# Performance work log

Measured on AMD Instinct MI355X. Metric: run time of the kernel, lower is better.

The kernel has to match this reference:

```python
import jax, jax.numpy as jnp
import numpy as np

NUM_HEADS = 8


def setup_inputs() -> dict:
    key = jax.random.key(0)
    ks = jax.random.split(key, 6)
    S, B, L, E = 4, 4, 4096, 1024
    scale = 1.0 / np.sqrt(E)
    return {
        "stream_outputs": jax.random.normal(ks[0], (S, B, L, E), dtype=jnp.float32),
        "stream_query": jax.random.normal(ks[1], (1, 1, E), dtype=jnp.float32),
        "in_proj_weight": jax.random.uniform(ks[2], (3 * E, E), dtype=jnp.float32, minval=-scale, maxval=scale),
        "in_proj_bias": jnp.zeros((3 * E,), dtype=jnp.float32),
        "out_proj_weight": jax.random.uniform(ks[3], (E, E), dtype=jnp.float32, minval=-scale, maxval=scale),
        "out_proj_bias": jnp.zeros((E,), dtype=jnp.float32),
    }


def reference(stream_outputs, stream_query, in_proj_weight, in_proj_bias,
              out_proj_weight, out_proj_bias):
    S, B, L, E = stream_outputs.shape
    H = NUM_HEADS
    D = E // H
    scale = 1.0 / jnp.sqrt(jnp.asarray(D, dtype=stream_outputs.dtype))

    Wq, Wk, Wv = in_proj_weight[:E], in_proj_weight[E:2 * E], in_proj_weight[2 * E:]
    bq, bk, bv = in_proj_bias[:E], in_proj_bias[E:2 * E], in_proj_bias[2 * E:]

    # query is identical for every token: project once -> [H, D]
    q = (stream_query[0, 0] @ Wq.T + bq).reshape(H, D)

    # streams as KV: [B, L, S, E]
    x = jnp.transpose(stream_outputs, (1, 2, 0, 3))
    k = (jnp.einsum('blse,fe->blsf', x, Wk) + bk).reshape(B, L, S, H, D)
    v = (jnp.einsum('blse,fe->blsf', x, Wv) + bv).reshape(B, L, S, H, D)

    logits = jnp.einsum('hd,blshd->blhs', q, k) * scale  # [B, L, H, S]
    attn = jax.nn.softmax(logits, axis=-1)

    ctx = jnp.einsum('blhs,blshd->blhd', attn, v).reshape(B, L, E)
    aggregated = jnp.einsum('ble,fe->blf', ctx, out_proj_weight) + out_proj_bias

    # torch MHA returns attn weights averaged over heads -> [B, L, S] -> [S, B, L]
    weights = jnp.transpose(jnp.mean(attn, axis=2), (2, 0, 1))
    return aggregated, weights
```

## Files before the change

kernel.cpp:

```cpp
#include <hip/hip_runtime.h>
#include <hip/hip_bf16.h>
#include <math.h>

#define SS 4
#define BB 4
#define LL 4096
#define EE 1024
#define HH 8
#define DD 128
#define TT (BB*LL)
#define AGG_ELEMS ((long)TT*EE)

using bf16  = __hip_bfloat16;
using bfp2  = __hip_bfloat162;
using bhalf8_t  = __attribute__((ext_vector_type(8))) short;
using floatx4_t = __attribute__((ext_vector_type(4))) float;

__device__ __forceinline__ void gload16(const void* g, void* l) {
  __builtin_amdgcn_global_load_lds((const __attribute__((address_space(1))) void*)g,
                                   (__attribute__((address_space(3))) void*)l, 16, 0, 0);
}

__global__ __launch_bounds__(256) void k_convert(const float* __restrict__ Wv,
                                                 const float* __restrict__ Wo,
                                                 bf16* __restrict__ WvB,
                                                 bf16* __restrict__ WoB) {
  int i = blockIdx.x * 256 + threadIdx.x;
  float4 a = ((const float4*)Wv)[i];
  float4 b = ((const float4*)Wo)[i];
  bfp2 p;
  p.x = __float2bfloat16(a.x); p.y = __float2bfloat16(a.y); ((bfp2*)WvB)[2*i]   = p;
  p.x = __float2bfloat16(a.z); p.y = __float2bfloat16(a.w); ((bfp2*)WvB)[2*i+1] = p;
  p.x = __float2bfloat16(b.x); p.y = __float2bfloat16(b.y); ((bfp2*)WoB)[2*i]   = p;
  p.x = __float2bfloat16(b.z); p.y = __float2bfloat16(b.w); ((bfp2*)WoB)[2*i+1] = p;
}

__global__ __launch_bounds__(256) void k_q(const float* __restrict__ query,
                                           const float* __restrict__ Wq,
                                           const float* __restrict__ bq,
                                           float* __restrict__ q) {
  int lane = threadIdx.x & 63;
  int f = blockIdx.x * 4 + (threadIdx.x >> 6);
  const float* wr = Wq + (long)f * EE;
  float acc = 0.f;
  for (int e = lane; e < EE; e += 64) acc += query[e] * wr[e];
#pragma unroll
  for (int o = 32; o; o >>= 1) acc += __shfl_down(acc, o);
  if (!lane) q[f] = acc + bq[f];
}

__global__ __launch_bounds__(256) void k_qk(const float* __restrict__ q,
                                            const float* __restrict__ Wk,
                                            float* __restrict__ qk) {
  int idx = blockIdx.x * 256 + threadIdx.x;
  int h = idx >> 10, e = idx & 1023;
  const float* qh = q + h * DD;
  float acc = 0.f;
  for (int d = 0; d < DD; ++d) acc += qh[d] * Wk[(long)(h * DD + d) * EE + e];
  qk[idx] = acc * 0.088388347648318447f;
}

__global__ __launch_bounds__(256) void k_attn_y(const float* __restrict__ X,
                                                const float* __restrict__ qk,
                                                float* __restrict__ attn_ws,
                                                float* __restrict__ wout,
                                                bf16* __restrict__ y,
                                                int h0, int hc, int doAttn) {
  __shared__ float xs[16][EE];
  int tid = threadIdx.x;
  long tok0 = (long)blockIdx.x * 4;
#pragma unroll
  for (int it = 0; it < 16; ++it) {
    int j = it * 256 + tid;
    int row = j >> 8, c4 = j & 255;
    long tok = tok0 + (row >> 2);
    int s = row & 3;
    const float4* src = (const float4*)(X + ((long)s * TT + tok) * EE) + c4;
    *(float4*)&xs[row][c4 * 4] = *src;
  }
  __syncthreads();

  int wave = tid >> 6, lane = tid & 63;
  long tok = tok0 + wave;
  int r0 = wave * 4;
  float attn[HH][SS];

  if (doAttn) {
    float acc[HH][SS];
#pragma unroll
    for (int h = 0; h < HH; ++h)
#pragma unroll
      for (int s = 0; s < SS; ++s) acc[h][s] = 0.f;
    for (int i = 0; i < 16; ++i) {
      int e = i * 64 + lane;
      float xv[SS];
#pragma unroll
      for (int s = 0; s < SS; ++s) xv[s] = xs[r0 + s][e];
#pragma unroll
      for (int h = 0; h < HH; ++h) {
        float qv = qk[h * EE + e];
#pragma unroll
        for (int s = 0; s < SS; ++s) acc[h][s] += qv * xv[s];
      }
    }
#pragma unroll
    for (int h = 0; h < HH; ++h)
#pragma unroll
      for (int s = 0; s < SS; ++s)
#pragma unroll
        for (int o = 1; o < 64; o <<= 1) acc[h][s] += __shfl_xor(acc[h][s], o);
#pragma unroll
    for (int h = 0; h < HH; ++h) {
      float m = fmaxf(fmaxf(acc[h][0], acc[h][1]), fmaxf(acc[h][2], acc[h][3]));
      float p0 = __expf(acc[h][0] - m), p1 = __expf(acc[h][1] - m);
      float p2 = __expf(acc[h][2] - m), p3 = __expf(acc[h][3] - m);
      float inv = 1.f / (p0 + p1 + p2 + p3);
      attn[h][0] = p0 * inv; attn[h][1] = p1 * inv;
      attn[h][2] = p2 * inv; attn[h][3] = p3 * inv;
    }
    if (lane == 0) {
#pragma unroll
      for (int h = 0; h < HH; ++h)
#pragma unroll
        for (int s = 0; s < SS; ++s) attn_ws[tok * 32 + h * 4 + s] = attn[h][s];
#pragma unroll
      for (int s = 0; s < SS; ++s) {
        float wsum = 0.125f * (attn[0][s] + attn[1][s] + attn[2][s] + attn[3][s] +
                               attn[4][s] + attn[5][s] + attn[6][s] + attn[7][s]);
        wout[(long)s * TT + tok] = wsum;
      }
    }
  } else {
#pragma unroll
    for (int h = 0; h < HH; ++h)
#pragma unroll
      for (int s = 0; s < SS; ++s) attn[h][s] = attn_ws[tok * 32 + h * 4 + s];
  }

#pragma unroll
  for (int h = 0; h < HH; ++h) {
    if (h < h0 || h >= h0 + hc) continue;
    float a0 = attn[h][0], a1 = attn[h][1], a2 = attn[h][2], a3 = attn[h][3];
    bf16* yr = y + ((long)(h - h0) * TT + tok) * EE;
#pragma unroll
    for (int i = 0; i < 8; ++i) {
      int e = i * 128 + lane * 2;
      float2 v0 = *(const float2*)&xs[r0][e];
      float2 v1 = *(const float2*)&xs[r0 + 1][e];
      float2 v2 = *(const float2*)&xs[r0 + 2][e];
      float2 v3 = *(const float2*)&xs[r0 + 3][e];
      float u0 = a0 * v0.x + a1 * v1.x + a2 * v2.x + a3 * v3.x;
      float u1 = a0 * v0.y + a1 * v1.y + a2 * v2.y + a3 * v3.y;
      bfp2 pk; pk.x = __float2bfloat16(u0); pk.y = __float2bfloat16(u1);
      *(bfp2*)&yr[e] = pk;
    }
  }
}

template <bool OUTF32>
__global__ __launch_bounds__(256) void k_gemm128(const bf16* __restrict__ A,
                                                 const bf16* __restrict__ Bt,
                                                 const float* __restrict__ bias,
                                                 void* __restrict__ C,
                                                 int K, int ldc, int nbase0,
                                                 long aStrideY, long btStrideY) {
  __shared__ bf16 As[128 * 64];
  __shared__ bf16 Bs[128 * 64];
  A  += (long)blockIdx.y * aStrideY;
  Bt += (long)blockIdx.y * btStrideY;
  int tid = threadIdx.x, wave = tid >> 6, lane = tid & 63;
  long m0 = (long)blockIdx.x * 128;
  int wm = wave >> 1, wn = wave & 1;
  floatx4_t acc[4][4];
#pragma unroll
  for (int i = 0; i < 4; ++i)
#pragma unroll
    for (int j = 0; j < 4; ++j) acc[i][j] = (floatx4_t){0.f, 0.f, 0.f, 0.f};

  int lrow = lane >> 3;
  int lcol = (lane & 7) * 8;

  for (int k0 = 0; k0 < K; k0 += 64) {
#pragma unroll
    for (int i = 0; i < 4; ++i) {
      int seg = wave * 4 + i;
      int row = seg * 8 + lrow;
      gload16(A  + (m0 + row) * (long)K + k0 + lcol, &As[seg * 512]);
      gload16(Bt + (long)row * K        + k0 + lcol, &Bs[seg * 512]);
    }
    __syncthreads();
#pragma unroll
    for (int kk = 0; kk < 2; ++kk) {
      bhalf8_t af[4], bfr[4];
#pragma unroll
      for (int mi = 0; mi < 4; ++mi) {
        int m = wm * 64 + mi * 16 + (lane & 15);
        af[mi] = *(const bhalf8_t*)&As[m * 64 + kk * 32 + (lane >> 4) * 8];
      }
#pragma unroll
      for (int ni = 0; ni < 4; ++ni) {
        int n = wn * 64 + ni * 16 + (lane & 15);
        bfr[ni] = *(const bhalf8_t*)&Bs[n * 64 + kk * 32 + (lane >> 4) * 8];
      }
#pragma unroll
      for (int mi = 0; mi < 4; ++mi)
#pragma unroll
        for (int ni = 0; ni < 4; ++ni)
          acc[mi][ni] = __builtin_amdgcn_mfma_f32_16x16x32_bf16(af[mi], bfr[ni], acc[mi][ni], 0, 0, 0);
    }
    __syncthreads();
  }

  int cl = lane & 15, rg = (lane >> 4) * 4;
#pragma unroll
  for (int mi = 0; mi < 4; ++mi) {
    long trow = m0 + wm * 64 + mi * 16 + rg;
#pragma unroll
    for (int ni = 0; ni < 4; ++ni) {
      int n = nbase0 + blockIdx.y * 128 + wn * 64 + ni * 16 + cl;
      float bv = bias[n];
#pragma unroll
      for (int r = 0; r < 4; ++r) {
        float v = acc[mi][ni][r] + bv;
        if (OUTF32) ((float*)C)[(trow + r) * (long)ldc + n] = v;
        else        ((bf16*)C)[(trow + r) * (long)ldc + n] = __float2bfloat16(v);
      }
    }
  }
}

extern "C" void kernel_launch(void* const* d_in, const int* in_sizes, int n_in,
                              void* d_out, int out_size, void* d_ws, size_t ws_size,
                              hipStream_t stream) {
  const float* SO  = (const float*)d_in[0];
  const float* SQ  = (const float*)d_in[1];
  const float* IPW = (const float*)d_in[2];
  const float* IPB = (const float*)d_in[3];
  const float* OPW = (const float*)d_in[4];
  const float* OPB = (const float*)d_in[5];
  float* out = (float*)d_out;
  char* ws = (char*)d_ws;

  size_t off = 0;
  auto alloc = [&](size_t bytes) -> void* {
    void* p = ws + off;
    off = (off + bytes + 255) & ~(size_t)255;
    return p;
  };
  float* q    = (float*)alloc((size_t)EE * 4);
  float* qk   = (float*)alloc((size_t)HH * EE * 4);
  float* attn = (float*)alloc((size_t)TT * 32 * 4);
  bf16*  WvB  = (bf16*) alloc((size_t)EE * EE * 2);
  bf16*  WoB  = (bf16*) alloc((size_t)EE * EE * 2);
  bf16*  ctxB = (bf16*) alloc((size_t)TT * EE * 2);
  int HC = HH;
  while (HC > 1 && off + (size_t)TT * HC * EE * 2 > ws_size) HC >>= 1;
  bf16* y = (bf16*)(ws + off);

  k_convert<<<EE * EE / 1024, 256, 0, stream>>>(IPW + 2 * EE * EE, OPW, WvB, WoB);
  k_q<<<EE / 4, 256, 0, stream>>>(SQ, IPW, IPB, q);
  k_qk<<<HH * EE / 256, 256, 0, stream>>>(q, IPW + EE * EE, qk);

  for (int h0 = 0; h0 < HH; h0 += HC) {
    k_attn_y<<<TT / 4, 256, 0, stream>>>(SO, qk, attn, out + AGG_ELEMS, y, h0, HC, h0 == 0 ? 1 : 0);
    k_gemm128<false><<<dim3(TT / 128, HC), 256, 0, stream>>>(
        y, WvB + (long)h0 * DD * EE, IPB + 2 * EE, ctxB,
        EE, EE, h0 * DD, (long)TT * EE, (long)DD * EE);
  }
  k_gemm128<true><<<dim3(TT / 128, HH), 256, 0, stream>>>(
      ctxB, WoB, OPB, out, EE, EE, 0, 0L, (long)DD * EE);
}
```

Before: 610.9 us.

## Fuse attention-weighted value projection and output projection into one kernel

Splits attention weight computation into a standalone kernel that keeps qk in shared memory. The per-head weighted stream mixing, V projection and output projection are fused into one 512-thread kernel per 64-token tile. Inside it, X chunks are double-buffered into LDS, the mixed bf16 values and ctx stay on chip, and B operands are read directly from global memory. This removes the large y and ctx intermediates and the extra GEMM launches. In exchange it uses a large LDS footprint, gets low occupancy with only 256 blocks, and has unstaged weight loads.

New measurement: 659.3 us. 1.08x slower.

```diff
diff --git a/kernel.cpp b/kernel.cpp
--- a/kernel.cpp
+++ b/kernel.cpp
@@ -15,6 +15,7 @@
 using bfp2  = __hip_bfloat162;
 using bhalf8_t  = __attribute__((ext_vector_type(8))) short;
 using floatx4_t = __attribute__((ext_vector_type(4))) float;
+using ushort8_t = __attribute__((ext_vector_type(8))) unsigned short;
 
 __device__ __forceinline__ void gload16(const void* g, void* l) {
   __builtin_amdgcn_global_load_lds((const __attribute__((address_space(1))) void*)g,
@@ -60,173 +61,203 @@
   qk[idx] = acc * 0.088388347648318447f;
 }
 
-__global__ __launch_bounds__(256) void k_attn_y(const float* __restrict__ X,
-                                                const float* __restrict__ qk,
-                                                float* __restrict__ attn_ws,
-                                                float* __restrict__ wout,
-                                                bf16* __restrict__ y,
-                                                int h0, int hc, int doAttn) {
-  __shared__ float xs[16][EE];
-  int tid = threadIdx.x;
-  long tok0 = (long)blockIdx.x * 4;
-#pragma unroll
-  for (int it = 0; it < 16; ++it) {
-    int j = it * 256 + tid;
-    int row = j >> 8, c4 = j & 255;
-    long tok = tok0 + (row >> 2);
-    int s = row & 3;
-    const float4* src = (const float4*)(X + ((long)s * TT + tok) * EE) + c4;
-    *(float4*)&xs[row][c4 * 4] = *src;
-  }
+__global__ __launch_bounds__(256) void k_attn(const float* __restrict__ X,
+                                              const float* __restrict__ qk,
+                                              float* __restrict__ attn_ws,
+                                              float* __restrict__ wout) {
+  __shared__ float qs[HH * EE];
+#pragma unroll
+  for (int i = 0; i < 8; ++i)
+    ((float4*)qs)[i * 256 + threadIdx.x] = ((const float4*)qk)[i * 256 + threadIdx.x];
   __syncthreads();
-
-  int wave = tid >> 6, lane = tid & 63;
-  long tok = tok0 + wave;
-  int r0 = wave * 4;
-  float attn[HH][SS];
-
-  if (doAttn) {
-    float acc[HH][SS];
-#pragma unroll
-    for (int h = 0; h < HH; ++h)
-#pragma unroll
-      for (int s = 0; s < SS; ++s) acc[h][s] = 0.f;
-    for (int i = 0; i < 16; ++i) {
-      int e = i * 64 + lane;
-      float xv[SS];
-#pragma unroll
-      for (int s = 0; s < SS; ++s) xv[s] = xs[r0 + s][e];
-#pragma unroll
-      for (int h = 0; h < HH; ++h) {
-        float qv = qk[h * EE + e];
-#pragma unroll
-        for (int s = 0; s < SS; ++s) acc[h][s] += qv * xv[s];
-      }
-    }
-#pragma unroll
-    for (int h = 0; h < HH; ++h)
+  int lane = threadIdx.x & 63;
+  long tok = (long)blockIdx.x * 4 + (threadIdx.x >> 6);
+  float acc[HH][SS];
+#pragma unroll
+  for (int h = 0; h < HH; ++h)
+#pragma unroll
+    for (int s = 0; s < SS; ++s) acc[h][s] = 0.f;
+#pragma unroll
+  for (int it = 0; it < 4; ++it) {
+    int e0 = it * 256 + lane * 4;
+    float4 xv[SS];
+#pragma unroll
+    for (int s = 0; s < SS; ++s)
+      xv[s] = *(const float4*)&X[((long)s * TT + tok) * EE + e0];
+#pragma unroll
+    for (int h = 0; h < HH; ++h) {
+      float4 qv = *(const float4*)&qs[h * EE + e0];
 #pragma unroll
       for (int s = 0; s < SS; ++s)
-#pragma unroll
-        for (int o = 1; o < 64; o <<= 1) acc[h][s] += __shfl_xor(acc[h][s], o);
+        acc[h][s] += qv.x * xv[s].x + qv.y * xv[s].y + qv.z * xv[s].z + qv.w * xv[s].w;
+    }
+  }
+#pragma unroll
+  for (int h = 0; h < HH; ++h)
+#pragma unroll
+    for (int s = 0; s < SS; ++s)
+#pragma unroll
+      for (int o = 1; o < 64; o <<= 1) acc[h][s] += __shfl_xor(acc[h][s], o);
+  if (lane == 0) {
+    float aw[HH][SS];
 #pragma unroll
     for (int h = 0; h < HH; ++h) {
       float m = fmaxf(fmaxf(acc[h][0], acc[h][1]), fmaxf(acc[h][2], acc[h][3]));
       float p0 = __expf(acc[h][0] - m), p1 = __expf(acc[h][1] - m);
       float p2 = __expf(acc[h][2] - m), p3 = __expf(acc[h][3] - m);
       float inv = 1.f / (p0 + p1 + p2 + p3);
-      attn[h][0] = p0 * inv; attn[h][1] = p1 * inv;
-      attn[h][2] = p2 * inv; attn[h][3] = p3 * inv;
-    }
-    if (lane == 0) {
-#pragma unroll
-      for (int h = 0; h < HH; ++h)
-#pragma unroll
-        for (int s = 0; s < SS; ++s) attn_ws[tok * 32 + h * 4 + s] = attn[h][s];
-#pragma unroll
-      for (int s = 0; s < SS; ++s) {
-        float wsum = 0.125f * (attn[0][s] + attn[1][s] + attn[2][s] + attn[3][s] +
-                               attn[4][s] + attn[5][s] + attn[6][s] + attn[7][s]);
-        wout[(long)s * TT + tok] = wsum;
-      }
-    }
-  } else {
-#pragma unroll
-    for (int h = 0; h < HH; ++h)
-#pragma unroll
-      for (int s = 0; s < SS; ++s) attn[h][s] = attn_ws[tok * 32 + h * 4 + s];
-  }
-
-#pragma unroll
-  for (int h = 0; h < HH; ++h) {
-    if (h < h0 || h >= h0 + hc) continue;
-    float a0 = attn[h][0], a1 = attn[h][1], a2 = attn[h][2], a3 = attn[h][3];
-    bf16* yr = y + ((long)(h - h0) * TT + tok) * EE;
-#pragma unroll
-    for (int i = 0; i < 8; ++i) {
-      int e = i * 128 + lane * 2;
-      float2 v0 = *(const float2*)&xs[r0][e];
-      float2 v1 = *(const float2*)&xs[r0 + 1][e];
-      float2 v2 = *(const float2*)&xs[r0 + 2][e];
-      float2 v3 = *(const float2*)&xs[r0 + 3][e];
-      float u0 = a0 * v0.x + a1 * v1.x + a2 * v2.x + a3 * v3.x;
-      float u1 = a0 * v0.y + a1 * v1.y + a2 * v2.y + a3 * v3.y;
-      bfp2 pk; pk.x = __float2bfloat16(u0); pk.y = __float2bfloat16(u1);
-      *(bfp2*)&yr[e] = pk;
-    }
-  }
-}
-
-template <bool OUTF32>
-__global__ __launch_bounds__(256) void k_gemm128(const bf16* __restrict__ A,
-                                                 const bf16* __restrict__ Bt,
-                                                 const float* __restrict__ bias,
-                                                 void* __restrict__ C,
-                                                 int K, int ldc, int nbase0,
-                                                 long aStrideY, long btStrideY) {
-  __shared__ bf16 As[128 * 64];
-  __shared__ bf16 Bs[128 * 64];
-  A  += (long)blockIdx.y * aStrideY;
-  Bt += (long)blockIdx.y * btStrideY;
-  int tid = threadIdx.x, wave = tid >> 6, lane = tid & 63;
-  long m0 = (long)blockIdx.x * 128;
-  int wm = wave >> 1, wn = wave & 1;
-  floatx4_t acc[4][4];
-#pragma unroll
-  for (int i = 0; i < 4; ++i)
-#pragma unroll
-    for (int j = 0; j < 4; ++j) acc[i][j] = (floatx4_t){0.f, 0.f, 0.f, 0.f};
-
-  int lrow = lane >> 3;
-  int lcol = (lane & 7) * 8;
-
-  for (int k0 = 0; k0 < K; k0 += 64) {
+      aw[h][0] = p0 * inv; aw[h][1] = p1 * inv; aw[h][2] = p2 * inv; aw[h][3] = p3 * inv;
+      *(float4*)&attn_ws[tok * 32 + h * 4] = (float4){aw[h][0], aw[h][1], aw[h][2], aw[h][3]};
+    }
+#pragma unroll
+    for (int s = 0; s < SS; ++s) {
+      float wsum = 0.125f * (aw[0][s] + aw[1][s] + aw[2][s] + aw[3][s] +
+                             aw[4][s] + aw[5][s] + aw[6][s] + aw[7][s]);
+      wout[(long)s * TT + tok] = wsum;
+    }
+  }
+}
+
+__global__ __launch_bounds__(512, 2) void k_fused(const float* __restrict__ X,
+                                                  const float* __restrict__ attn_g,
+                                                  const bf16* __restrict__ WvB,
+                                                  const bf16* __restrict__ WoB,
+                                                  const float* __restrict__ bvp,
+                                                  const float* __restrict__ bop,
+                                                  float* __restrict__ out) {
+  union SMem {
+    struct { float xs[2][8192]; unsigned short yb[16384]; } p1;
+    unsigned short ctx[65536];
+  };
+  __shared__ SMem sm;
+  const int tid = threadIdx.x;
+  const int w = tid >> 6, lane = tid & 63;
+  const int tk = lane & 15, hi = lane >> 4;
+  const long t0 = (long)blockIdx.x * 64;
+  const int ty = tid >> 3, e4 = tid & 3, hh = (tid >> 2) & 1;
+
+  float4 a4[4];
+#pragma unroll
+  for (int j = 0; j < 4; ++j)
+    a4[j] = *(const float4*)&attn_g[(t0 + ty) * 32 + hh * 16 + j * 4];
+
+  floatx4_t acc[4][8];
+#pragma unroll
+  for (int mi = 0; mi < 4; ++mi)
+#pragma unroll
+    for (int ni = 0; ni < 8; ++ni) acc[mi][ni] = (floatx4_t){0.f, 0.f, 0.f, 0.f};
+
+  auto stage = [&](int c, int buf) {
+    float* dst = sm.p1.xs[buf];
 #pragma unroll
     for (int i = 0; i < 4; ++i) {
-      int seg = wave * 4 + i;
-      int row = seg * 8 + lrow;
-      gload16(A  + (m0 + row) * (long)K + k0 + lcol, &As[seg * 512]);
-      gload16(Bt + (long)row * K        + k0 + lcol, &Bs[seg * 512]);
+      int aa = i * 8 + w;
+      int r = aa * 8 + (lane >> 3);
+      int s = r >> 6, t = r & 63;
+      int g = (lane & 7) ^ (t & 7);
+      gload16(X + ((long)s * TT + t0 + t) * EE + c * 32 + g * 4, dst + aa * 256);
+    }
+  };
+
+  stage(0, 0);
+  __syncthreads();
+
+  for (int c = 0; c < 32; ++c) {
+    const float* xsc = sm.p1.xs[c & 1];
+    float4 xlo[4], xhi[4];
+#pragma unroll
+    for (int s = 0; s < 4; ++s) {
+      int row = s * 64 + ty;
+      xlo[s] = *(const float4*)&xsc[row * 32 + (((2 * e4) ^ (ty & 7)) * 4)];
+      xhi[s] = *(const float4*)&xsc[row * 32 + (((2 * e4 + 1) ^ (ty & 7)) * 4)];
+    }
+#pragma unroll
+    for (int j = 0; j < 4; ++j) {
+      int h = hh * 4 + j;
+      float u[8];
+#pragma unroll
+      for (int k = 0; k < 4; ++k) {
+        u[k]     = a4[j].x * ((&xlo[0].x)[k]) + a4[j].y * ((&xlo[1].x)[k]) +
+                   a4[j].z * ((&xlo[2].x)[k]) + a4[j].w * ((&xlo[3].x)[k]);
+        u[k + 4] = a4[j].x * ((&xhi[0].x)[k]) + a4[j].y * ((&xhi[1].x)[k]) +
+                   a4[j].z * ((&xhi[2].x)[k]) + a4[j].w * ((&xhi[3].x)[k]);
+      }
+      ushort8_t o;
+#pragma unroll
+      for (int k = 0; k < 8; ++k) {
+        bf16 b = __float2bfloat16(u[k]);
+        o[k] = *(unsigned short*)&b;
+      }
+      *(ushort8_t*)&sm.p1.yb[(h * 64 + ty) * 32 + ((e4 ^ ((ty >> 1) & 3)) * 8)] = o;
     }
     __syncthreads();
+    if (c + 1 < 32) stage(c + 1, (c + 1) & 1);
+    bhalf8_t af[4];
+#pragma unroll
+    for (int mi = 0; mi < 4; ++mi) {
+      int t = mi * 16 + tk;
+      af[mi] = *(const bhalf8_t*)&sm.p1.yb[(w * 64 + t) * 32 + ((hi ^ ((t >> 1) & 3)) * 8)];
+    }
+#pragma unroll
+    for (int ni = 0; ni < 8; ++ni) {
+      bhalf8_t bfr = *(const bhalf8_t*)&WvB[(long)(w * 128 + ni * 16 + tk) * EE + c * 32 + hi * 8];
+#pragma unroll
+      for (int mi = 0; mi < 4; ++mi)
+        acc[mi][ni] = __builtin_amdgcn_mfma_f32_16x16x32_bf16(af[mi], bfr, acc[mi][ni], 0, 0, 0);
+    }
+    __syncthreads();
+  }
+
+#pragma unroll
+  for (int mi = 0; mi < 4; ++mi)
+#pragma unroll
+    for (int ni = 0; ni < 8; ++ni) {
+      int f = w * 128 + ni * 16 + tk;
+      float bv = bvp[f];
+#pragma unroll
+      for (int r = 0; r < 4; ++r) {
+        int t = mi * 16 + hi * 4 + r;
+        bf16 b = __float2bfloat16(acc[mi][ni][r] + bv);
+        sm.ctx[t * 1024 + (f >> 6) * 64 + ((((f >> 3) & 7) ^ (t & 7)) * 8) + (f & 7)] =
+            *(unsigned short*)&b;
+      }
+    }
+  __syncthreads();
+
+#pragma unroll
+  for (int mi = 0; mi < 4; ++mi)
+#pragma unroll
+    for (int ni = 0; ni < 8; ++ni) acc[mi][ni] = (floatx4_t){0.f, 0.f, 0.f, 0.f};
+  for (int c2 = 0; c2 < 16; ++c2) {
 #pragma unroll
     for (int kk = 0; kk < 2; ++kk) {
-      bhalf8_t af[4], bfr[4];
+      bhalf8_t af2[4];
 #pragma unroll
       for (int mi = 0; mi < 4; ++mi) {
-        int m = wm * 64 + mi * 16 + (lane & 15);
-        af[mi] = *(const bhalf8_t*)&As[m * 64 + kk * 32 + (lane >> 4) * 8];
-      }
-#pragma unroll
-      for (int ni = 0; ni < 4; ++ni) {
-        int n = wn * 64 + ni * 16 + (lane & 15);
-        bfr[ni] = *(const bhalf8_t*)&Bs[n * 64 + kk * 32 + (lane >> 4) * 8];
-      }
-#pragma unroll
-      for (int mi = 0; mi < 4; ++mi)
-#pragma unroll
-        for (int ni = 0; ni < 4; ++ni)
-          acc[mi][ni] = __builtin_amdgcn_mfma_f32_16x16x32_bf16(af[mi], bfr[ni], acc[mi][ni], 0, 0, 0);
-    }
-    __syncthreads();
-  }
-
-  int cl = lane & 15, rg = (lane >> 4) * 4;
-#pragma unroll
-  for (int mi = 0; mi < 4; ++mi) {
-    long trow = m0 + wm * 64 + mi * 16 + rg;
-#pragma unroll
-    for (int ni = 0; ni < 4; ++ni) {
-      int n = nbase0 + blockIdx.y * 128 + wn * 64 + ni * 16 + cl;
-      float bv = bias[n];
+        int t = mi * 16 + tk;
+        af2[mi] = *(const bhalf8_t*)&sm.ctx[t * 1024 + c2 * 64 + (((kk * 4 + hi) ^ (t & 7)) * 8)];
+      }
+#pragma unroll
+      for (int ni = 0; ni < 8; ++ni) {
+        bhalf8_t bfr = *(const bhalf8_t*)&WoB[(long)(w * 128 + ni * 16 + tk) * EE + c2 * 64 + kk * 32 + hi * 8];
+#pragma unroll
+        for (int mi = 0; mi < 4; ++mi)
+          acc[mi][ni] = __builtin_amdgcn_mfma_f32_16x16x32_bf16(af2[mi], bfr, acc[mi][ni], 0, 0, 0);
+      }
+    }
+  }
+#pragma unroll
+  for (int mi = 0; mi < 4; ++mi)
+#pragma unroll
+    for (int ni = 0; ni < 8; ++ni) {
+      int f = w * 128 + ni * 16 + tk;
+      float bo = bop[f];
 #pragma unroll
       for (int r = 0; r < 4; ++r) {
-        float v = acc[mi][ni][r] + bv;
-        if (OUTF32) ((float*)C)[(trow + r) * (long)ldc + n] = v;
-        else        ((bf16*)C)[(trow + r) * (long)ldc + n] = __float2bfloat16(v);
-      }
-    }
-  }
+        int t = mi * 16 + hi * 4 + r;
+        out[(t0 + t) * EE + f] = acc[mi][ni][r] + bo;
+      }
+    }
 }
 
 extern "C" void kernel_launch(void* const* d_in, const int* in_sizes, int n_in,
@@ -252,21 +283,10 @@
   float* attn = (float*)alloc((size_t)TT * 32 * 4);
   bf16*  WvB  = (bf16*) alloc((size_t)EE * EE * 2);
   bf16*  WoB  = (bf16*) alloc((size_t)EE * EE * 2);
-  bf16*  ctxB = (bf16*) alloc((size_t)TT * EE * 2);
-  int HC = HH;
-  while (HC > 1 && off + (size_t)TT * HC * EE * 2 > ws_size) HC >>= 1;
-  bf16* y = (bf16*)(ws + off);
 
   k_convert<<<EE * EE / 1024, 256, 0, stream>>>(IPW + 2 * EE * EE, OPW, WvB, WoB);
   k_q<<<EE / 4, 256, 0, stream>>>(SQ, IPW, IPB, q);
   k_qk<<<HH * EE / 256, 256, 0, stream>>>(q, IPW + EE * EE, qk);
-
-  for (int h0 = 0; h0 < HH; h0 += HC) {
-    k_attn_y<<<TT / 4, 256, 0, stream>>>(SO, qk, attn, out + AGG_ELEMS, y, h0, HC, h0 == 0 ? 1 : 0);
-    k_gemm128<false><<<dim3(TT / 128, HC), 256, 0, stream>>>(
-        y, WvB + (long)h0 * DD * EE, IPB + 2 * EE, ctxB,
-        EE, EE, h0 * DD, (long)TT * EE, (long)DD * EE);
-  }
-  k_gemm128<true><<<dim3(TT / 128, HH), 256, 0, stream>>>(
-      ctxB, WoB, OPB, out, EE, EE, 0, 0L, (long)DD * EE);
-}
+  k_attn<<<TT / 4, 256, 0, stream>>>(SO, qk, attn, out + AGG_ELEMS);
+  k_fused<<<TT / 64, 512, 0, stream>>>(SO, attn, WvB, WoB, IPB + 2 * EE, OPB, out);
+}
```
